# Kernel optimization log

Measured on AMD Instinct MI355X. Metric: run time of the kernel, lower is better.

The kernel has to match this reference:

```python
import jax, jax.numpy as jnp
import numpy as np

N = 65536    # collocation points
N1 = 1024    # RBF centers
EPS = 0.1    # multiscale parameter used for width init scale


def setup_inputs() -> dict:
    key = jax.random.key(0)
    ks = jax.random.split(key, 10)
    x = jax.random.uniform(ks[0], (N, 2), dtype=jnp.float32)

    def mk(i):
        h = jax.random.uniform(ks[3 * i + 1], (N1,), dtype=jnp.float32)
        c = jax.random.uniform(ks[3 * i + 2], (N1, 2), dtype=jnp.float32)
        w = 5.0 * jax.random.uniform(ks[3 * i + 3], (N1, 2), dtype=jnp.float32) / EPS
        return h, c, w

    h1, c1, w1 = mk(0)
    h2, c2, w2 = mk(1)
    h3, c3, w3 = mk(2)
    return dict(x=x, hight=h1, center=c1, width=w1,
                hight2=h2, center2=c2, width2=w2,
                hight3=h3, center3=c3, width3=w3)


def _rbf(X, c, h, w):
    """Gaussian RBF expansion. X:(N,2) points, c:(N1,2) centers,
    h:(N1,) heights, w:(N1,2) widths. Returns u, du/dx, du/dy, each (N,)."""
    x1 = X[:, 0:1] - c[None, :, 0]          # (N, N1)
    y1 = X[:, 1:2] - c[None, :, 1]          # (N, N1)
    d1 = w[:, 0] ** 2                        # (N1,)
    d2 = w[:, 1] ** 2                        # (N1,)
    e = jnp.exp(-(x1 ** 2) * d1 - (y1 ** 2) * d2)  # (N, N1)
    u = e @ h                                # (N,)
    ux = (-2.0 * x1 * d1 * e) @ h            # (N,)
    uy = (-2.0 * y1 * d2 * e) @ h            # (N,)
    return u, ux, uy


def reference(x, hight, center, width, hight2, center2, width2,
              hight3, center3, width3):
    _, ux, uy = _rbf(x, center, hight, width)
    P, Px, _ = _rbf(x, center2, hight2, width2)
    Q, _, Qy = _rbf(x, center3, hight3, width3)
    return (ux, uy, P, Px, Q, Qy)
```

## Files before the change

### kernel.cpp

```cpp
#include <hip/hip_runtime.h>
#include <math.h>

#define N_PTS  65536
#define N_CTR  1024
#define CHUNK  128
#define PPT    4
#define PPB    (256 * PPT)
#define LOG2E  1.4426950408889634f

#if __has_builtin(__builtin_amdgcn_exp2f)
#define EXP2(v) __builtin_amdgcn_exp2f(v)
#else
#define EXP2(v) exp2f(v)
#endif

__global__ __launch_bounds__(256) void srbf_main(
    const float* __restrict__ x,
    const float* __restrict__ h0, const float* __restrict__ c0, const float* __restrict__ w0,
    const float* __restrict__ h1, const float* __restrict__ c1, const float* __restrict__ w1,
    const float* __restrict__ h2, const float* __restrict__ c2, const float* __restrict__ w2,
    float* __restrict__ out)
{
    __shared__ float4 sA[CHUNK];
    __shared__ float4 sK[CHUNK];
    __shared__ float  sk3[CHUNK];

    const int bid   = blockIdx.x;
    const int set   = bid >> 9;
    const int r     = bid & 511;
    const int chunk = r >> 6;
    const int pblk  = r & 63;
    const int tid   = threadIdx.x;

    if (tid < CHUNK) {
        const int j = chunk * CHUNK + tid;
        const float*  h = (set == 0) ? h0 : ((set == 1) ? h1 : h2);
        const float2* c = (const float2*)((set == 0) ? c0 : ((set == 1) ? c1 : c2));
        const float2* w = (const float2*)((set == 0) ? w0 : ((set == 1) ? w1 : w2));
        float2 cj = c[j];
        float2 wj = w[j];
        float  hh = h[j];
        float d1 = wj.x * wj.x;
        float d2 = wj.y * wj.y;
        float zb =  2.f * cj.x * d1 * LOG2E;
        float zc = -d1 * LOG2E;
        float zd =  2.f * cj.y * d2 * LOG2E;
        float ze = -d2 * LOG2E;
        float za = -(cj.x * cj.x * d1 + cj.y * cj.y * d2) * LOG2E;
        float k0, k1, k2, k3;
        if (set == 0) {
            k0 = -2.f * hh * d1;  k1 = 2.f * hh * d1 * cj.x;
            k2 = -2.f * hh * d2;  k3 = 2.f * hh * d2 * cj.y;
        } else if (set == 1) {
            k0 = hh;  k1 = -2.f * hh * d1;  k2 = 2.f * hh * d1 * cj.x;  k3 = 0.f;
        } else {
            k0 = hh;  k1 = -2.f * hh * d2;  k2 = 2.f * hh * d2 * cj.y;  k3 = 0.f;
        }
        sA[tid]  = make_float4(zb, zc, zd, ze);
        sK[tid]  = make_float4(za, k0, k1, k2);
        sk3[tid] = k3;
    }

    const int base = pblk * PPB + tid;
    float X[PPT], Y[PPT];
    #pragma unroll
    for (int p = 0; p < PPT; ++p) {
        float2 q = ((const float2*)x)[base + p * 256];
        X[p] = q.x;  Y[p] = q.y;
    }
    __syncthreads();

    if (set == 0) {
        float A0[PPT], A1[PPT], A2[PPT], A3[PPT];
        #pragma unroll
        for (int p = 0; p < PPT; ++p) { A0[p] = A1[p] = A2[p] = A3[p] = 0.f; }

        #pragma unroll 4
        for (int j = 0; j < CHUNK; ++j) {
            const float4 A  = sA[j];
            const float4 K  = sK[j];
            const float  k3 = sk3[j];
            float e[PPT];
            #pragma unroll
            for (int p = 0; p < PPT; ++p) {
                float t1 = fmaf(X[p], A.y, A.x);
                float t2 = fmaf(X[p], t1,  K.x);
                float t3 = fmaf(Y[p], A.w, A.z);
                float s  = fmaf(Y[p], t3,  t2);
                e[p] = EXP2(s);
            }
            #pragma unroll
            for (int p = 0; p < PPT; ++p) {
                A0[p] = fmaf(K.y, e[p], A0[p]);
                A1[p] = fmaf(K.z, e[p], A1[p]);
                A2[p] = fmaf(K.w, e[p], A2[p]);
                A3[p] = fmaf(k3,  e[p], A3[p]);
            }
        }
        #pragma unroll
        for (int p = 0; p < PPT; ++p) {
            const int i = base + p * 256;
            atomicAdd(&out[i],         fmaf(X[p], A0[p], A1[p]));
            atomicAdd(&out[N_PTS + i], fmaf(Y[p], A2[p], A3[p]));
        }
    } else {
        float A0[PPT], A1[PPT], A2[PPT];
        #pragma unroll
        for (int p = 0; p < PPT; ++p) { A0[p] = A1[p] = A2[p] = 0.f; }

        #pragma unroll 4
        for (int j = 0; j < CHUNK; ++j) {
            const float4 A = sA[j];
            const float4 K = sK[j];
            float e[PPT];
            #pragma unroll
            for (int p = 0; p < PPT; ++p) {
                float t1 = fmaf(X[p], A.y, A.x);
                float t2 = fmaf(X[p], t1,  K.x);
                float t3 = fmaf(Y[p], A.w, A.z);
                float s  = fmaf(Y[p], t3,  t2);
                e[p] = EXP2(s);
            }
            #pragma unroll
            for (int p = 0; p < PPT; ++p) {
                A0[p] = fmaf(K.y, e[p], A0[p]);
                A1[p] = fmaf(K.z, e[p], A1[p]);
                A2[p] = fmaf(K.w, e[p], A2[p]);
            }
        }
        float* o = out + (size_t)set * 2 * N_PTS;
        #pragma unroll
        for (int p = 0; p < PPT; ++p) {
            const int i = base + p * 256;
            const float g = (set == 1) ? X[p] : Y[p];
            atomicAdd(&o[i],         A0[p]);
            atomicAdd(&o[N_PTS + i], fmaf(g, A1[p], A2[p]));
        }
    }
}

extern "C" void kernel_launch(void* const* d_in, const int* in_sizes, int n_in,
                              void* d_out, int out_size, void* d_ws, size_t ws_size,
                              hipStream_t stream) {
    const float* x  = (const float*)d_in[0];
    const float* h1 = (const float*)d_in[1];
    const float* c1 = (const float*)d_in[2];
    const float* w1 = (const float*)d_in[3];
    const float* h2 = (const float*)d_in[4];
    const float* c2 = (const float*)d_in[5];
    const float* w2 = (const float*)d_in[6];
    const float* h3 = (const float*)d_in[7];
    const float* c3 = (const float*)d_in[8];
    const float* w3 = (const float*)d_in[9];

    hipMemsetAsync(d_out, 0, (size_t)out_size * sizeof(float), stream);

    srbf_main<<<dim3(1536), dim3(256), 0, stream>>>(
        x, h1, c1, w1, h2, c2, w2, h3, c3, w3, (float*)d_out);
}
```

Baseline: 52.27 us.

## Bin points into spatial cells and skip RBF centers beyond a Gaussian cutoff

Adds a bucketing pass that sorts the collocation points into a 16x16 grid of cells, with an overflow list for cells holding more than 256 points. Each main block then handles one cell and one RBF set. It keeps only the centers whose Gaussian exponent at the nearest point of the cell stays above a 2^-40 cutoff, compacting them into LDS with ballot and popcount. Outputs are written directly instead of through a memset and atomics. The aim is to skip the exp work for far, negligible centers, at the cost of extra launches, one point per thread, imbalance across cells, and a small truncation error.

Result: slower. 79.09 us (+51.3%).

```diff
diff --git a/kernel.cpp b/kernel.cpp
--- a/kernel.cpp
+++ b/kernel.cpp
@@ -1,12 +1,14 @@
 #include <hip/hip_runtime.h>
 #include <math.h>
 
-#define N_PTS  65536
-#define N_CTR  1024
-#define CHUNK  128
-#define PPT    4
-#define PPB    (256 * PPT)
-#define LOG2E  1.4426950408889634f
+#define N_PTS   65536
+#define N_CTR   1024
+#define NCELLS  256
+#define SLOTS   256
+#define OCAP    4096
+#define CUT     40.0f
+#define LOG2E   1.4426950408889634f
+#define MAXL    (N_CTR + 16)
 
 #if __has_builtin(__builtin_amdgcn_exp2f)
 #define EXP2(v) __builtin_amdgcn_exp2f(v)
@@ -14,128 +16,253 @@
 #define EXP2(v) exp2f(v)
 #endif
 
+struct Fold { float4 A; float4 K; float k3; };
+
+__device__ __forceinline__ Fold fold_center(int set, float2 cj, float2 wj, float hh) {
+    float d1 = wj.x * wj.x, d2 = wj.y * wj.y;
+    Fold f;
+    f.A = make_float4(2.f * cj.x * d1 * LOG2E, -d1 * LOG2E,
+                      2.f * cj.y * d2 * LOG2E, -d2 * LOG2E);
+    float za = -(cj.x * cj.x * d1 + cj.y * cj.y * d2) * LOG2E;
+    float k0, k1, k2, k3;
+    if (set == 0) {
+        k0 = -2.f * hh * d1;  k1 = 2.f * hh * d1 * cj.x;
+        k2 = -2.f * hh * d2;  k3 = 2.f * hh * d2 * cj.y;
+    } else if (set == 1) {
+        k0 = hh;  k1 = -2.f * hh * d1;  k2 = 2.f * hh * d1 * cj.x;  k3 = 0.f;
+    } else {
+        k0 = hh;  k1 = -2.f * hh * d2;  k2 = 2.f * hh * d2 * cj.y;  k3 = 0.f;
+    }
+    f.K = make_float4(za, k0, k1, k2);
+    f.k3 = k3;
+    return f;
+}
+
+__global__ __launch_bounds__(256) void zero_kernel(unsigned int* __restrict__ cnt,
+                                                   unsigned int* __restrict__ ocnt) {
+    cnt[threadIdx.x] = 0u;
+    if (threadIdx.x == 0) *ocnt = 0u;
+}
+
+__global__ __launch_bounds__(256) void bucket_kernel(
+    const float* __restrict__ x, unsigned int* __restrict__ cnt,
+    unsigned short* __restrict__ idxl,
+    unsigned int* __restrict__ ocnt, unsigned short* __restrict__ olist)
+{
+    const int i = blockIdx.x * 256 + threadIdx.x;
+    float2 p = ((const float2*)x)[i];
+    int cx = (int)(p.x * 16.f); cx = cx > 15 ? 15 : (cx < 0 ? 0 : cx);
+    int cy = (int)(p.y * 16.f); cy = cy > 15 ? 15 : (cy < 0 ? 0 : cy);
+    const int cell = cy * 16 + cx;
+    unsigned int slot = atomicAdd(&cnt[cell], 1u);
+    if (slot < SLOTS) {
+        idxl[cell * SLOTS + slot] = (unsigned short)i;
+    } else {
+        unsigned int os = atomicAdd(ocnt, 1u);
+        if (os < OCAP) olist[os] = (unsigned short)i;
+    }
+}
+
 __global__ __launch_bounds__(256) void srbf_main(
     const float* __restrict__ x,
     const float* __restrict__ h0, const float* __restrict__ c0, const float* __restrict__ w0,
     const float* __restrict__ h1, const float* __restrict__ c1, const float* __restrict__ w1,
     const float* __restrict__ h2, const float* __restrict__ c2, const float* __restrict__ w2,
+    const unsigned int* __restrict__ cnt, const unsigned short* __restrict__ idxl,
     float* __restrict__ out)
 {
-    __shared__ float4 sA[CHUNK];
-    __shared__ float4 sK[CHUNK];
-    __shared__ float  sk3[CHUNK];
-
-    const int bid   = blockIdx.x;
-    const int set   = bid >> 9;
-    const int r     = bid & 511;
-    const int chunk = r >> 6;
-    const int pblk  = r & 63;
-    const int tid   = threadIdx.x;
-
-    if (tid < CHUNK) {
-        const int j = chunk * CHUNK + tid;
-        const float*  h = (set == 0) ? h0 : ((set == 1) ? h1 : h2);
-        const float2* c = (const float2*)((set == 0) ? c0 : ((set == 1) ? c1 : c2));
-        const float2* w = (const float2*)((set == 0) ? w0 : ((set == 1) ? w1 : w2));
-        float2 cj = c[j];
-        float2 wj = w[j];
+    __shared__ float4 sA[MAXL];
+    __shared__ float4 sK[MAXL];
+    __shared__ float  sk3[MAXL];
+    __shared__ int    wtot[4];
+
+    const int bid  = blockIdx.x;
+    const int set  = bid >> 8;
+    const int cell = bid & 255;
+    const int tid  = threadIdx.x;
+    const int lane = tid & 63;
+    const int wv   = tid >> 6;
+
+    const float*  h = (set == 0) ? h0 : ((set == 1) ? h1 : h2);
+    const float2* c = (const float2*)((set == 0) ? c0 : ((set == 1) ? c1 : c2));
+    const float2* w = (const float2*)((set == 0) ? w0 : ((set == 1) ? w1 : w2));
+
+    const float cx0 = (float)(cell & 15) * 0.0625f;
+    const float cy0 = (float)(cell >> 4) * 0.0625f;
+    const float cx1 = cx0 + 0.0625f;
+    const float cy1 = cy0 + 0.0625f;
+
+    bool lv[4];
+    Fold f[4];
+    unsigned long long mk[4];
+    #pragma unroll
+    for (int r = 0; r < 4; ++r) {
+        const int j = r * 256 + tid;
+        float2 cj = c[j], wj = w[j];
         float  hh = h[j];
-        float d1 = wj.x * wj.x;
-        float d2 = wj.y * wj.y;
-        float zb =  2.f * cj.x * d1 * LOG2E;
-        float zc = -d1 * LOG2E;
-        float zd =  2.f * cj.y * d2 * LOG2E;
-        float ze = -d2 * LOG2E;
-        float za = -(cj.x * cj.x * d1 + cj.y * cj.y * d2) * LOG2E;
-        float k0, k1, k2, k3;
-        if (set == 0) {
-            k0 = -2.f * hh * d1;  k1 = 2.f * hh * d1 * cj.x;
-            k2 = -2.f * hh * d2;  k3 = 2.f * hh * d2 * cj.y;
-        } else if (set == 1) {
-            k0 = hh;  k1 = -2.f * hh * d1;  k2 = 2.f * hh * d1 * cj.x;  k3 = 0.f;
-        } else {
-            k0 = hh;  k1 = -2.f * hh * d2;  k2 = 2.f * hh * d2 * cj.y;  k3 = 0.f;
-        }
-        sA[tid]  = make_float4(zb, zc, zd, ze);
-        sK[tid]  = make_float4(za, k0, k1, k2);
-        sk3[tid] = k3;
-    }
-
-    const int base = pblk * PPB + tid;
-    float X[PPT], Y[PPT];
-    #pragma unroll
-    for (int p = 0; p < PPT; ++p) {
-        float2 q = ((const float2*)x)[base + p * 256];
-        X[p] = q.x;  Y[p] = q.y;
-    }
-    __syncthreads();
-
+        float d1 = wj.x * wj.x, d2 = wj.y * wj.y;
+        float dxm = fmaxf(fmaxf(cx0 - cj.x, cj.x - cx1), 0.f);
+        float dym = fmaxf(fmaxf(cy0 - cj.y, cj.y - cy1), 0.f);
+        lv[r] = (dxm * dxm * d1 + dym * dym * d2) * LOG2E < CUT;
+        f[r] = fold_center(set, cj, wj, hh);
+    }
+    #pragma unroll
+    for (int r = 0; r < 4; ++r) mk[r] = __ballot(lv[r]);
+    int wsum = __popcll(mk[0]) + __popcll(mk[1]) + __popcll(mk[2]) + __popcll(mk[3]);
+    if (lane == 0) wtot[wv] = wsum;
+    __syncthreads();
+    int base = 0, m = 0;
+    #pragma unroll
+    for (int q2 = 0; q2 < 4; ++q2) {
+        int t = wtot[q2];
+        m += t;
+        if (q2 < wv) base += t;
+    }
+    const unsigned long long lt = (1ull << lane) - 1ull;
+    int roff = 0;
+    #pragma unroll
+    for (int r = 0; r < 4; ++r) {
+        if (lv[r]) {
+            int pos = base + roff + __popcll(mk[r] & lt);
+            sA[pos] = f[r].A; sK[pos] = f[r].K; sk3[pos] = f[r].k3;
+        }
+        roff += __popcll(mk[r]);
+    }
+    const int mPad = (m + 15) & ~15;
+    if (tid < mPad - m) {
+        sA[m + tid]  = make_float4(0.f, 0.f, 0.f, 0.f);
+        sK[m + tid]  = make_float4(0.f, 0.f, 0.f, 0.f);
+        sk3[m + tid] = 0.f;
+    }
+
+    const int n = min((int)cnt[cell], SLOTS);
+    const bool valid = tid < n;
+    int o = 0; float X = 0.5f, Y = 0.5f;
+    if (valid) {
+        o = idxl[cell * SLOTS + tid];
+        float2 p = ((const float2*)x)[o];
+        X = p.x; Y = p.y;
+    }
+    __syncthreads();
+
+    float A0 = 0.f, A1 = 0.f, A2 = 0.f, A3 = 0.f;
     if (set == 0) {
-        float A0[PPT], A1[PPT], A2[PPT], A3[PPT];
+        for (int t = 0; t < mPad; t += 16) {
+            #pragma unroll
+            for (int u = 0; u < 16; ++u) {
+                float4 A = sA[t + u]; float4 K = sK[t + u]; float k3 = sk3[t + u];
+                float t1 = fmaf(X, A.y, A.x);
+                float t2 = fmaf(X, t1,  K.x);
+                float t3 = fmaf(Y, A.w, A.z);
+                float s  = fmaf(Y, t3,  t2);
+                float e  = EXP2(s);
+                A0 = fmaf(K.y, e, A0); A1 = fmaf(K.z, e, A1);
+                A2 = fmaf(K.w, e, A2); A3 = fmaf(k3,  e, A3);
+            }
+        }
+    } else {
+        for (int t = 0; t < mPad; t += 16) {
+            #pragma unroll
+            for (int u = 0; u < 16; ++u) {
+                float4 A = sA[t + u]; float4 K = sK[t + u];
+                float t1 = fmaf(X, A.y, A.x);
+                float t2 = fmaf(X, t1,  K.x);
+                float t3 = fmaf(Y, A.w, A.z);
+                float s  = fmaf(Y, t3,  t2);
+                float e  = EXP2(s);
+                A0 = fmaf(K.y, e, A0); A1 = fmaf(K.z, e, A1);
+                A2 = fmaf(K.w, e, A2);
+            }
+        }
+    }
+
+    if (valid) {
+        float* ob = out + (size_t)set * 2 * N_PTS;
+        float r1, r2;
+        if (set == 0)      { r1 = fmaf(X, A0, A1); r2 = fmaf(Y, A2, A3); }
+        else if (set == 1) { r1 = A0;              r2 = fmaf(X, A1, A2); }
+        else               { r1 = A0;              r2 = fmaf(Y, A1, A2); }
+        ob[o]         = r1;
+        ob[N_PTS + o] = r2;
+    }
+}
+
+__global__ __launch_bounds__(256) void overflow_kernel(
+    const float* __restrict__ x,
+    const float* __restrict__ h0, const float* __restrict__ c0, const float* __restrict__ w0,
+    const float* __restrict__ h1, const float* __restrict__ c1, const float* __restrict__ w1,
+    const float* __restrict__ h2, const float* __restrict__ c2, const float* __restrict__ w2,
+    const unsigned int* __restrict__ ocnt, const unsigned short* __restrict__ olist,
+    float* __restrict__ out)
+{
+    __shared__ float4 sA[N_CTR];
+    __shared__ float4 sK[N_CTR];
+    __shared__ float  sk3[N_CTR];
+    __shared__ float  red[4][64][4];
+
+    const int bid = blockIdx.x;
+    const int set = bid >> 6;
+    const int blk = bid & 63;
+    const int tid = threadIdx.x;
+    const int lane = tid & 63;
+    const int q    = tid >> 6;
+
+    int oc = (int)*ocnt;
+    oc = oc < OCAP ? oc : OCAP;
+    const int pbase = blk * 64;
+    if (pbase >= oc) return;
+
+    const float*  h = (set == 0) ? h0 : ((set == 1) ? h1 : h2);
+    const float2* c = (const float2*)((set == 0) ? c0 : ((set == 1) ? c1 : c2));
+    const float2* w = (const float2*)((set == 0) ? w0 : ((set == 1) ? w1 : w2));
+
+    #pragma unroll
+    for (int r = 0; r < 4; ++r) {
+        const int j = r * 256 + tid;
+        Fold f = fold_center(set, c[j], w[j], h[j]);
+        sA[j] = f.A; sK[j] = f.K; sk3[j] = f.k3;
+    }
+    __syncthreads();
+
+    const bool valid = (pbase + lane) < oc;
+    int o = 0; float X = 0.5f, Y = 0.5f;
+    if (valid) {
+        o = olist[pbase + lane];
+        float2 p = ((const float2*)x)[o];
+        X = p.x; Y = p.y;
+    }
+
+    float A0 = 0.f, A1 = 0.f, A2 = 0.f, A3 = 0.f;
+    const int cb = q * 256;
+    for (int t = 0; t < 256; t += 8) {
         #pragma unroll
-        for (int p = 0; p < PPT; ++p) { A0[p] = A1[p] = A2[p] = A3[p] = 0.f; }
-
-        #pragma unroll 4
-        for (int j = 0; j < CHUNK; ++j) {
-            const float4 A  = sA[j];
-            const float4 K  = sK[j];
-            const float  k3 = sk3[j];
-            float e[PPT];
-            #pragma unroll
-            for (int p = 0; p < PPT; ++p) {
-                float t1 = fmaf(X[p], A.y, A.x);
-                float t2 = fmaf(X[p], t1,  K.x);
-                float t3 = fmaf(Y[p], A.w, A.z);
-                float s  = fmaf(Y[p], t3,  t2);
-                e[p] = EXP2(s);
-            }
-            #pragma unroll
-            for (int p = 0; p < PPT; ++p) {
-                A0[p] = fmaf(K.y, e[p], A0[p]);
-                A1[p] = fmaf(K.z, e[p], A1[p]);
-                A2[p] = fmaf(K.w, e[p], A2[p]);
-                A3[p] = fmaf(k3,  e[p], A3[p]);
-            }
-        }
-        #pragma unroll
-        for (int p = 0; p < PPT; ++p) {
-            const int i = base + p * 256;
-            atomicAdd(&out[i],         fmaf(X[p], A0[p], A1[p]));
-            atomicAdd(&out[N_PTS + i], fmaf(Y[p], A2[p], A3[p]));
-        }
-    } else {
-        float A0[PPT], A1[PPT], A2[PPT];
-        #pragma unroll
-        for (int p = 0; p < PPT; ++p) { A0[p] = A1[p] = A2[p] = 0.f; }
-
-        #pragma unroll 4
-        for (int j = 0; j < CHUNK; ++j) {
-            const float4 A = sA[j];
-            const float4 K = sK[j];
-            float e[PPT];
-            #pragma unroll
-            for (int p = 0; p < PPT; ++p) {
-                float t1 = fmaf(X[p], A.y, A.x);
-                float t2 = fmaf(X[p], t1,  K.x);
-                float t3 = fmaf(Y[p], A.w, A.z);
-                float s  = fmaf(Y[p], t3,  t2);
-                e[p] = EXP2(s);
-            }
-            #pragma unroll
-            for (int p = 0; p < PPT; ++p) {
-                A0[p] = fmaf(K.y, e[p], A0[p]);
-                A1[p] = fmaf(K.z, e[p], A1[p]);
-                A2[p] = fmaf(K.w, e[p], A2[p]);
-            }
-        }
-        float* o = out + (size_t)set * 2 * N_PTS;
-        #pragma unroll
-        for (int p = 0; p < PPT; ++p) {
-            const int i = base + p * 256;
-            const float g = (set == 1) ? X[p] : Y[p];
-            atomicAdd(&o[i],         A0[p]);
-            atomicAdd(&o[N_PTS + i], fmaf(g, A1[p], A2[p]));
-        }
+        for (int u = 0; u < 8; ++u) {
+            float4 A = sA[cb + t + u]; float4 K = sK[cb + t + u]; float k3 = sk3[cb + t + u];
+            float t1 = fmaf(X, A.y, A.x);
+            float t2 = fmaf(X, t1,  K.x);
+            float t3 = fmaf(Y, A.w, A.z);
+            float s  = fmaf(Y, t3,  t2);
+            float e  = EXP2(s);
+            A0 = fmaf(K.y, e, A0); A1 = fmaf(K.z, e, A1);
+            A2 = fmaf(K.w, e, A2); A3 = fmaf(k3,  e, A3);
+        }
+    }
+    red[q][lane][0] = A0; red[q][lane][1] = A1;
+    red[q][lane][2] = A2; red[q][lane][3] = A3;
+    __syncthreads();
+
+    if (q == 0 && valid) {
+        A0 = red[0][lane][0] + red[1][lane][0] + red[2][lane][0] + red[3][lane][0];
+        A1 = red[0][lane][1] + red[1][lane][1] + red[2][lane][1] + red[3][lane][1];
+        A2 = red[0][lane][2] + red[1][lane][2] + red[2][lane][2] + red[3][lane][2];
+        A3 = red[0][lane][3] + red[1][lane][3] + red[2][lane][3] + red[3][lane][3];
+        float* ob = out + (size_t)set * 2 * N_PTS;
+        float r1, r2;
+        if (set == 0)      { r1 = fmaf(X, A0, A1); r2 = fmaf(Y, A2, A3); }
+        else if (set == 1) { r1 = A0;              r2 = fmaf(X, A1, A2); }
+        else               { r1 = A0;              r2 = fmaf(Y, A1, A2); }
+        ob[o]         = r1;
+        ob[N_PTS + o] = r2;
     }
 }
 
@@ -153,8 +280,19 @@
     const float* c3 = (const float*)d_in[8];
     const float* w3 = (const float*)d_in[9];
 
-    hipMemsetAsync(d_out, 0, (size_t)out_size * sizeof(float), stream);
-
-    srbf_main<<<dim3(1536), dim3(256), 0, stream>>>(
-        x, h1, c1, w1, h2, c2, w2, h3, c3, w3, (float*)d_out);
-}
+    char* ws = (char*)d_ws;
+    unsigned int*   cnt   = (unsigned int*)(ws);
+    unsigned int*   ocnt  = (unsigned int*)(ws + 1024);
+    unsigned short* olist = (unsigned short*)(ws + 2048);
+    unsigned short* idxl  = (unsigned short*)(ws + 10240);
+
+    zero_kernel<<<dim3(1), dim3(256), 0, stream>>>(cnt, ocnt);
+
+    bucket_kernel<<<dim3(256), dim3(256), 0, stream>>>(x, cnt, idxl, ocnt, olist);
+
+    srbf_main<<<dim3(768), dim3(256), 0, stream>>>(
+        x, h1, c1, w1, h2, c2, w2, h3, c3, w3, cnt, idxl, (float*)d_out);
+
+    overflow_kernel<<<dim3(192), dim3(256), 0, stream>>>(
+        x, h1, c1, w1, h2, c2, w2, h3, c3, w3, ocnt, olist, (float*)d_out);
+}
```
